# Kernel optimization log

Hardware: AMD Instinct MI355X
Metric: run time of the kernel (lower is better)

The kernel has to match this reference:

```python
import jax, jax.numpy as jnp
import numpy as np

B, S, HID = 2, 2048, 2048
NH, NKV, D = 32, 4, 64
N_REP = NH // NKV
EPS = 1e-6
ROPE_THETA = 10000.0


def _rotate_half(x):
    h = x.shape[-1] // 2
    return jnp.concatenate([-x[..., h:], x[..., :h]], axis=-1)


def _rmsnorm(x, gamma):
    # RMSNorm over last dim (head_dim)
    return x * jax.lax.rsqrt(jnp.mean(x * x, axis=-1, keepdims=True) + EPS) * gamma


def setup_inputs() -> dict:
    key = jax.random.key(0)
    ks = jax.random.split(key, 8)
    hidden_states = jax.random.normal(ks[0], (B, S, HID), dtype=jnp.float32)
    # rotary cos/sin tables, shape [B, S, D]
    pos = jnp.arange(S, dtype=jnp.float32)
    inv_freq = 1.0 / (ROPE_THETA ** (jnp.arange(0, D, 2, dtype=jnp.float32) / D))
    freqs = pos[:, None] * inv_freq[None, :]            # [S, D/2]
    emb = jnp.concatenate([freqs, freqs], axis=-1)      # [S, D]
    cos = jnp.broadcast_to(jnp.cos(emb)[None], (B, S, D))
    sin = jnp.broadcast_to(jnp.sin(emb)[None], (B, S, D))
    sc = 0.02
    Wq = jax.random.normal(ks[1], (NH * D, HID), dtype=jnp.float32) * sc
    Wk = jax.random.normal(ks[2], (NKV * D, HID), dtype=jnp.float32) * sc
    Wv = jax.random.normal(ks[3], (NKV * D, HID), dtype=jnp.float32) * sc
    Wg = jax.random.normal(ks[4], (NH * D, HID), dtype=jnp.float32) * sc
    Wo = jax.random.normal(ks[5], (HID, NH * D), dtype=jnp.float32) * sc
    q_gamma = jnp.ones((D,), dtype=jnp.float32)
    k_gamma = jnp.ones((D,), dtype=jnp.float32)
    return dict(hidden_states=hidden_states, cos=cos, sin=sin,
                Wq=Wq, Wk=Wk, Wv=Wv, Wg=Wg, Wo=Wo,
                q_gamma=q_gamma, k_gamma=k_gamma)


def reference(hidden_states, cos, sin, Wq, Wk, Wv, Wg, Wo, q_gamma, k_gamma):
    b, s, _ = hidden_states.shape
    q = (hidden_states @ Wq.T).reshape(b, s, NH, D)
    k = (hidden_states @ Wk.T).reshape(b, s, NKV, D)
    v = (hidden_states @ Wv.T).reshape(b, s, NKV, D)
    gate = hidden_states @ Wg.T                       # [B, S, NH*D]
    # per-head RMSNorm on q/k
    q = _rmsnorm(q, q_gamma)
    k = _rmsnorm(k, k_gamma)
    # [B, H, S, D]
    q = q.transpose(0, 2, 1, 3)
    k = k.transpose(0, 2, 1, 3)
    v = v.transpose(0, 2, 1, 3)
    # RoPE (unsqueeze_dim=1)
    c = cos[:, None, :, :]
    sn = sin[:, None, :, :]
    q = q * c + _rotate_half(q) * sn
    k = k * c + _rotate_half(k) * sn
    # GQA: repeat kv heads
    kr = jnp.repeat(k, N_REP, axis=1)
    vr = jnp.repeat(v, N_REP, axis=1)
    scaling = D ** -0.5
    scores = jnp.einsum('bhqd,bhkd->bhqk', q, kr) * scaling
    w = jax.nn.softmax(scores.astype(jnp.float32), axis=-1).astype(q.dtype)
    out = jnp.einsum('bhqk,bhkd->bhqd', w, vr)
    out = out.transpose(0, 2, 1, 3).reshape(b, s, NH * D)
    out = out * jax.nn.sigmoid(gate)
    return out @ Wo.T
```

## Files before the change

kernel.cpp:

```cpp
#include <hip/hip_runtime.h>


#define LOG2E 1.44269504088896340736f

typedef __attribute__((ext_vector_type(4))) float f32x4;
typedef __attribute__((ext_vector_type(8))) short bf16x8;

__device__ __forceinline__ float bf2f(unsigned short u) {
  union { unsigned u; float f; } x; x.u = ((unsigned)u) << 16; return x.f;
}
__device__ __forceinline__ unsigned short f2bf(float f) {
  union { float f; unsigned u; } x; x.f = f;
  unsigned r = x.u + 0x7fffu + ((x.u >> 16) & 1u);
  return (unsigned short)(r >> 16);
}

__device__ __forceinline__ void async16(void* lds, const void* g) {
  __builtin_amdgcn_global_load_lds(
      (const __attribute__((address_space(1))) unsigned*)g,
      (__attribute__((address_space(3))) unsigned*)lds, 16, 0, 0);
}
__device__ __forceinline__ void lds_fence() {
  __asm__ volatile("s_waitcnt lgkmcnt(0)" ::: "memory");
}

__global__ __launch_bounds__(256) void cvt_all(
    const float* __restrict__ s0, const float* __restrict__ s1,
    const float* __restrict__ s2, const float* __restrict__ s3,
    const float* __restrict__ s4, const float* __restrict__ s5,
    unsigned short* __restrict__ d0, unsigned short* __restrict__ d1,
    unsigned short* __restrict__ d2, unsigned short* __restrict__ d3,
    unsigned short* __restrict__ d4, unsigned short* __restrict__ d5) {
  long i = (long)blockIdx.x * 256 + threadIdx.x;
  const float* s; unsigned short* d; long off;
  if      (i < 2097152) { s = s0; d = d0; off = 0; }
  else if (i < 3145728) { s = s1; d = d1; off = 2097152; }
  else if (i < 3276800) { s = s2; d = d2; off = 3145728; }
  else if (i < 3407872) { s = s3; d = d3; off = 3276800; }
  else if (i < 4456448) { s = s4; d = d4; off = 3407872; }
  else                  { s = s5; d = d5; off = 4456448; }
  long j = i - off;
  float4 v = reinterpret_cast<const float4*>(s)[j];
  ushort4 u;
  u.x = f2bf(v.x); u.y = f2bf(v.y); u.z = f2bf(v.z); u.w = f2bf(v.w);
  reinterpret_cast<ushort4*>(d)[j] = u;
}

template <typename CT>
__device__ __forceinline__ void gemm128(
    const unsigned short* __restrict__ A, const unsigned short* __restrict__ W,
    CT* __restrict__ C, int m0, int n0, int ldc, int K,
    unsigned short* As, unsigned short* Bs) {
  const int tid = threadIdx.x;
  const int w = tid >> 6, l = tid & 63, quad = l >> 4, l16 = l & 15;
  const int wm = (w & 1) * 64, wn = (w >> 1) * 64;

  f32x4 acc[4][4];
  const f32x4 Z4 = {0.f, 0.f, 0.f, 0.f};
#pragma unroll
  for (int i = 0; i < 4; i++)
#pragma unroll
    for (int j = 0; j < 4; j++) acc[i][j] = Z4;

  const int srow = tid >> 2;
  const int scol = (tid & 3) * 8;
  const unsigned short* gA = A + (size_t)(m0 + srow) * K + scol;
  const unsigned short* gB = W + (size_t)(n0 + srow) * K + scol;
  unsigned short* lA = As + tid * 8;
  unsigned short* lB = Bs + tid * 8;

  for (int kb = 0; kb < K; kb += 32) {
    async16(lA,        gA + kb);
    async16(lA + 2048, gA + (size_t)64 * K + kb);
    async16(lB,        gB + kb);
    async16(lB + 2048, gB + (size_t)64 * K + kb);
    __syncthreads();

    bf16x8 af[4], bf[4];
#pragma unroll
    for (int mt = 0; mt < 4; mt++)
      af[mt] = *(const bf16x8*)&As[(wm + mt * 16 + l16) * 32 + quad * 8];
#pragma unroll
    for (int nt = 0; nt < 4; nt++)
      bf[nt] = *(const bf16x8*)&Bs[(wn + nt * 16 + l16) * 32 + quad * 8];
#pragma unroll
    for (int mt = 0; mt < 4; mt++)
#pragma unroll
      for (int nt = 0; nt < 4; nt++)
        acc[mt][nt] = __builtin_amdgcn_mfma_f32_16x16x32_bf16(
            af[mt], bf[nt], acc[mt][nt], 0, 0, 0);
    __syncthreads();
  }

#pragma unroll
  for (int mt = 0; mt < 4; mt++)
#pragma unroll
    for (int nt = 0; nt < 4; nt++) {
      int row = m0 + wm + mt * 16 + quad * 4;
      int col = n0 + wn + nt * 16 + l16;
#pragma unroll
      for (int r = 0; r < 4; r++) {
        if constexpr (sizeof(CT) == 2)
          C[(size_t)(row + r) * ldc + col] = f2bf(acc[mt][nt][r]);
        else
          C[(size_t)(row + r) * ldc + col] = acc[mt][nt][r];
      }
    }
}

__global__ __launch_bounds__(256) void gemm_qkvg(
    const unsigned short* __restrict__ X,
    const unsigned short* __restrict__ Wq, const unsigned short* __restrict__ Wk,
    const unsigned short* __restrict__ Wv, const unsigned short* __restrict__ Wg,
    unsigned short* __restrict__ Qr, unsigned short* __restrict__ Kr,
    unsigned short* __restrict__ Vr, unsigned short* __restrict__ Gr) {
  __shared__ __attribute__((aligned(16))) unsigned short As[128 * 32];
  __shared__ __attribute__((aligned(16))) unsigned short Bs[128 * 32];
  int ny = blockIdx.y;
  const unsigned short* W; unsigned short* C; int n0, ldc;
  if (ny < 16)      { W = Wq; C = Qr; n0 = ny * 128;        ldc = 2048; }
  else if (ny < 18) { W = Wk; C = Kr; n0 = (ny - 16) * 128; ldc = 256;  }
  else if (ny < 20) { W = Wv; C = Vr; n0 = (ny - 18) * 128; ldc = 256;  }
  else              { W = Wg; C = Gr; n0 = (ny - 20) * 128; ldc = 2048; }
  gemm128<unsigned short>(X, W, C, blockIdx.x * 128, n0, ldc, 2048, As, Bs);
}

__global__ __launch_bounds__(256) void gemm_out_k(
    const unsigned short* __restrict__ A, const unsigned short* __restrict__ W,
    float* __restrict__ C) {
  __shared__ __attribute__((aligned(16))) unsigned short As[128 * 32];
  __shared__ __attribute__((aligned(16))) unsigned short Bs[128 * 32];
  gemm128<float>(A, W, C, blockIdx.x * 128, blockIdx.y * 128, 2048, 2048, As, Bs);
}

__global__ __launch_bounds__(256) void prep_qkv(
    const unsigned short* __restrict__ Qr, const unsigned short* __restrict__ Kr,
    const unsigned short* __restrict__ Vr,
    const float* __restrict__ cosb, const float* __restrict__ sinb,
    const float* __restrict__ qg, const float* __restrict__ kg,
    unsigned short* __restrict__ Qn, unsigned short* __restrict__ Kn,
    unsigned short* __restrict__ Vt) {
  int idx = blockIdx.x * 4 + (threadIdx.x >> 6);
  int d = threadIdx.x & 63;
  int token = idx / 40;
  int unit = idx - token * 40;
  int b = token >> 11, s = token & 2047;

  if (unit >= 36) {
    int kvh = unit - 36;
    Vt[((size_t)(b * 4 + kvh) * 64 + d) * 2048 + s] =
        Vr[(size_t)token * 256 + kvh * 64 + d];
    return;
  }
  const unsigned short* src; const float* gamma; float scale; unsigned short* dst;
  if (unit < 32) {
    src = Qr + (size_t)token * 2048 + unit * 64;
    gamma = qg; scale = 0.125f;
    dst = Qn + ((size_t)(b * 32 + unit) * 2048 + s) * 64;
  } else {
    int kvh = unit - 32;
    src = Kr + (size_t)token * 256 + kvh * 64;
    gamma = kg; scale = LOG2E;
    dst = Kn + ((size_t)(b * 4 + kvh) * 2048 + s) * 64;
  }
  float x = bf2f(src[d]);
  float ss = x * x;
#pragma unroll
  for (int off = 32; off >= 1; off >>= 1) ss += __shfl_xor(ss, off);
  float rr = rsqrtf(ss * (1.0f / 64.0f) + 1e-6f);
  float xn = x * rr * gamma[d];
  float other = __shfl_xor(xn, 32);
  float rot = (d < 32) ? -other : other;
  size_t cs = (size_t)(b * 2048 + s) * 64 + d;
  dst[d] = f2bf((xn * cosb[cs] + rot * sinb[cs]) * scale);
}

__global__ __launch_bounds__(256, 4) void attn(
    const unsigned short* __restrict__ Qn, const unsigned short* __restrict__ Kn,
    const unsigned short* __restrict__ Vt, const unsigned short* __restrict__ gate,
    unsigned short* __restrict__ act) {
  __shared__ __attribute__((aligned(16))) unsigned short smem[20480];
  unsigned short* Ps = smem + 16384;

  const int tid = threadIdx.x, w = tid >> 6, l = tid & 63;
  const int quad = l >> 4, l16 = l & 15, l7 = l16 & 7;
  const int bh = blockIdx.y, b = bh >> 5, h = bh & 31, kvh = h >> 3;
  const int q0 = blockIdx.x * 128;

  const unsigned short* Qg = Qn + ((size_t)(b * 32 + h) * 2048 + q0) * 64;
  const unsigned short* Kg = Kn + (size_t)(b * 4 + kvh) * 2048 * 64;
  const unsigned short* Vg = Vt + (size_t)(b * 4 + kvh) * 64 * 2048;
  unsigned short* Pw = Ps + w * 1024;

  const int kq_src = ((tid & 7) ^ ((tid >> 3) & 7)) * 8;

#pragma unroll
  for (int i = 0; i < 4; i++)
    async16(smem + i * 2048 + tid * 8,
            Qg + (size_t)(i * 32 + (tid >> 3)) * 64 + kq_src);
  __syncthreads();
  bf16x8 qf[2][2];
#pragma unroll
  for (int mt = 0; mt < 2; mt++)
#pragma unroll
    for (int ks = 0; ks < 2; ks++) {
      int row = w * 32 + mt * 16 + l16;
      qf[mt][ks] = *(const bf16x8*)&smem[row * 64 + ((ks * 4 + quad) ^ l7) * 8];
    }
  __syncthreads();

  const f32x4 Z4 = {0.f, 0.f, 0.f, 0.f};
  f32x4 O[2][4];
  float lp[2][4];
#pragma unroll
  for (int mt = 0; mt < 2; mt++) {
#pragma unroll
    for (int nt = 0; nt < 4; nt++) O[mt][nt] = Z4;
#pragma unroll
    for (int r = 0; r < 4; r++) lp[mt][r] = 0.f;
  }

#pragma unroll
  for (int i = 0; i < 2; i++) {
    async16(smem + i * 2048 + tid * 8,
            Kg + (size_t)(i * 32 + (tid >> 3)) * 64 + kq_src);
    async16(smem + 4096 + i * 2048 + tid * 8,
            Vg + (size_t)(i * 32 + (tid >> 3)) * 2048 + kq_src);
  }

  for (int kt = 0; kt < 32; kt++) {
    __syncthreads();

    if (kt < 31) {
      unsigned short* nb = smem + ((kt + 1) & 1) * 8192;
      const int s1 = (kt + 1) * 64;
#pragma unroll
      for (int i = 0; i < 2; i++) {
        async16(nb + i * 2048 + tid * 8,
                Kg + (size_t)(s1 + i * 32 + (tid >> 3)) * 64 + kq_src);
        async16(nb + 4096 + i * 2048 + tid * 8,
                Vg + (size_t)(i * 32 + (tid >> 3)) * 2048 + s1 + kq_src);
      }
    }

    unsigned short* Ks  = smem + (kt & 1) * 8192;
    unsigned short* Vts = Ks + 4096;

    f32x4 sc[2][4];
#pragma unroll
    for (int mt = 0; mt < 2; mt++)
#pragma unroll
      for (int nt = 0; nt < 4; nt++) sc[mt][nt] = Z4;
#pragma unroll
    for (int nt = 0; nt < 4; nt++) {
      int row = nt * 16 + l16;
      bf16x8 kf0 = *(const bf16x8*)&Ks[row * 64 + (quad ^ l7) * 8];
      bf16x8 kf1 = *(const bf16x8*)&Ks[row * 64 + ((4 + quad) ^ l7) * 8];
#pragma unroll
      for (int mt = 0; mt < 2; mt++) {
        sc[mt][nt] = __builtin_amdgcn_mfma_f32_16x16x32_bf16(qf[mt][0], kf0, sc[mt][nt], 0, 0, 0);
        sc[mt][nt] = __builtin_amdgcn_mfma_f32_16x16x32_bf16(qf[mt][1], kf1, sc[mt][nt], 0, 0, 0);
      }
    }

#pragma unroll
    for (int ks2 = 0; ks2 < 2; ks2++) {
#pragma unroll
      for (int mt = 0; mt < 2; mt++)
#pragma unroll
        for (int ntl = 0; ntl < 2; ntl++) {
          int nt = ks2 * 2 + ntl;
#pragma unroll
          for (int r = 0; r < 4; r++) {
            float p = __builtin_amdgcn_exp2f(sc[mt][nt][r]);
            union { float f; unsigned u; } x; x.f = p;
            union { unsigned u; float f; } t; t.u = x.u & 0xffff0000u;
            lp[mt][r] += t.f;
            int q = mt * 16 + quad * 4 + r;
            int c = ntl * 2 + (l16 >> 3);
            int phys = c ^ ((q >> 1) & 3);
            Pw[q * 32 + phys * 8 + l7] = (unsigned short)(x.u >> 16);
          }
        }
      lds_fence();

      bf16x8 pf[2];
#pragma unroll
      for (int mt = 0; mt < 2; mt++) {
        int q = mt * 16 + l16;
        int phys = quad ^ ((l16 >> 1) & 3);
        pf[mt] = *(const bf16x8*)&Pw[q * 32 + phys * 8];
      }
#pragma unroll
      for (int nt2 = 0; nt2 < 4; nt2++) {
        int d = nt2 * 16 + l16;
        bf16x8 vf = *(const bf16x8*)&Vts[d * 64 + ((ks2 * 4 + quad) ^ l7) * 8];
#pragma unroll
        for (int mt = 0; mt < 2; mt++)
          O[mt][nt2] = __builtin_amdgcn_mfma_f32_16x16x32_bf16(
              pf[mt], vf, O[mt][nt2], 0, 0, 0);
      }
      lds_fence();
    }
  }

#pragma unroll
  for (int mt = 0; mt < 2; mt++)
#pragma unroll
    for (int r = 0; r < 4; r++) {
      float s = lp[mt][r];
#pragma unroll
      for (int off = 1; off < 16; off <<= 1) s += __shfl_xor(s, off);
      lp[mt][r] = s;
    }

#pragma unroll
  for (int mt = 0; mt < 2; mt++) {
    float inv[4];
#pragma unroll
    for (int r = 0; r < 4; r++) inv[r] = 1.0f / lp[mt][r];
#pragma unroll
    for (int nt = 0; nt < 4; nt++)
#pragma unroll
      for (int r = 0; r < 4; r++) {
        int srow = q0 + w * 32 + mt * 16 + quad * 4 + r;
        int col = h * 64 + nt * 16 + l16;
        size_t off = (size_t)(b * 2048 + srow) * 2048 + col;
        float g = bf2f(gate[off]);
        float sig = 1.0f / (1.0f + __builtin_amdgcn_exp2f(-g * LOG2E));
        act[off] = f2bf(O[mt][nt][r] * inv[r] * sig);
      }
  }
}

extern "C" void kernel_launch(void* const* d_in, const int* in_sizes, int n_in,
                              void* d_out, int out_size, void* d_ws, size_t ws_size,
                              hipStream_t stream) {
  const float* hid  = (const float*)d_in[0];
  const float* cosb = (const float*)d_in[1];
  const float* sinb = (const float*)d_in[2];
  const float* Wq   = (const float*)d_in[3];
  const float* Wk   = (const float*)d_in[4];
  const float* Wv   = (const float*)d_in[5];
  const float* Wg   = (const float*)d_in[6];
  const float* Wo   = (const float*)d_in[7];
  const float* qg   = (const float*)d_in[8];
  const float* kg   = (const float*)d_in[9];
  float* out = (float*)d_out;

  char* ws = (char*)d_ws;
  unsigned short* Xb   = (unsigned short*)(ws);
  unsigned short* WqB  = (unsigned short*)(ws + 16777216);
  unsigned short* WkB  = (unsigned short*)(ws + 25165824);
  unsigned short* WvB  = (unsigned short*)(ws + 26214400);
  unsigned short* WgB  = (unsigned short*)(ws + 27262976);
  unsigned short* WoB  = (unsigned short*)(ws + 35651584);
  unsigned short* Qraw = (unsigned short*)(ws + 44040192);
  unsigned short* Kraw = (unsigned short*)(ws + 60817408);
  unsigned short* Vraw = (unsigned short*)(ws + 62914560);
  unsigned short* gate = (unsigned short*)(ws + 65011712);
  unsigned short* Kn   = (unsigned short*)(ws + 81788928);
  unsigned short* Vt   = (unsigned short*)(ws + 83886080);
  unsigned short* Qn  = Xb;
  unsigned short* act = WqB;

  cvt_all<<<dim3(21504), dim3(256), 0, stream>>>(
      hid, Wq, Wk, Wv, Wg, Wo, Xb, WqB, WkB, WvB, WgB, WoB);

  gemm_qkvg<<<dim3(32, 36), dim3(256), 0, stream>>>(
      Xb, WqB, WkB, WvB, WgB, Qraw, Kraw, Vraw, gate);

  prep_qkv<<<dim3(40960), dim3(256), 0, stream>>>(
      Qraw, Kraw, Vraw, cosb, sinb, qg, kg, Qn, Kn, Vt);

  attn<<<dim3(16, 64), dim3(256), 0, stream>>>(Qn, Kn, Vt, gate, act);

  gemm_out_k<<<dim3(32, 16), dim3(256), 0, stream>>>(act, WoB, out);
}
```

Before: 411.3 us.

## Fuse RMSNorm, RoPE and V transpose into QKVG GEMM epilogue; swizzle LDS

Removes the separate prep_qkv kernel. The QKVG GEMM epilogue now applies per-head RMSNorm, RoPE and scaling to Q/K, writes V already transposed, and writes gate directly, using 16-lane shuffles inside the MFMA tile. This drops a full round trip of raw Q/K/V through global memory and one kernel launch. It also XOR-swizzles the LDS column layout in the shared GEMM mainloop to reduce bank conflicts. In exchange, the epilogue writes to the transposed V with scattered, strided stores, and it adds per-element cos/sin loads.

```diff
diff --git a/kernel.cpp b/kernel.cpp
--- a/kernel.cpp
+++ b/kernel.cpp
@@ -46,16 +46,14 @@
   reinterpret_cast<ushort4*>(d)[j] = u;
 }
 
-template <typename CT>
-__device__ __forceinline__ void gemm128(
+__device__ __forceinline__ void gemm_main(
     const unsigned short* __restrict__ A, const unsigned short* __restrict__ W,
-    CT* __restrict__ C, int m0, int n0, int ldc, int K,
-    unsigned short* As, unsigned short* Bs) {
+    int m0, int n0, int K, unsigned short* As, unsigned short* Bs,
+    f32x4 acc[4][4]) {
   const int tid = threadIdx.x;
   const int w = tid >> 6, l = tid & 63, quad = l >> 4, l16 = l & 15;
   const int wm = (w & 1) * 64, wn = (w >> 1) * 64;
 
-  f32x4 acc[4][4];
   const f32x4 Z4 = {0.f, 0.f, 0.f, 0.f};
 #pragma unroll
   for (int i = 0; i < 4; i++)
@@ -63,11 +61,12 @@
     for (int j = 0; j < 4; j++) acc[i][j] = Z4;
 
   const int srow = tid >> 2;
-  const int scol = (tid & 3) * 8;
+  const int scol = (((tid & 3) ^ ((tid >> 3) & 3))) * 8;
   const unsigned short* gA = A + (size_t)(m0 + srow) * K + scol;
   const unsigned short* gB = W + (size_t)(n0 + srow) * K + scol;
   unsigned short* lA = As + tid * 8;
   unsigned short* lB = Bs + tid * 8;
+  const int fsw = (quad ^ ((l16 >> 1) & 3)) * 8;
 
   for (int kb = 0; kb < K; kb += 32) {
     async16(lA,        gA + kb);
@@ -79,10 +78,10 @@
     bf16x8 af[4], bf[4];
 #pragma unroll
     for (int mt = 0; mt < 4; mt++)
-      af[mt] = *(const bf16x8*)&As[(wm + mt * 16 + l16) * 32 + quad * 8];
+      af[mt] = *(const bf16x8*)&As[(wm + mt * 16 + l16) * 32 + fsw];
 #pragma unroll
     for (int nt = 0; nt < 4; nt++)
-      bf[nt] = *(const bf16x8*)&Bs[(wn + nt * 16 + l16) * 32 + quad * 8];
+      bf[nt] = *(const bf16x8*)&Bs[(wn + nt * 16 + l16) * 32 + fsw];
 #pragma unroll
     for (int mt = 0; mt < 4; mt++)
 #pragma unroll
@@ -91,38 +90,100 @@
             af[mt], bf[nt], acc[mt][nt], 0, 0, 0);
     __syncthreads();
   }
-
-#pragma unroll
-  for (int mt = 0; mt < 4; mt++)
-#pragma unroll
-    for (int nt = 0; nt < 4; nt++) {
-      int row = m0 + wm + mt * 16 + quad * 4;
-      int col = n0 + wn + nt * 16 + l16;
-#pragma unroll
-      for (int r = 0; r < 4; r++) {
-        if constexpr (sizeof(CT) == 2)
-          C[(size_t)(row + r) * ldc + col] = f2bf(acc[mt][nt][r]);
-        else
-          C[(size_t)(row + r) * ldc + col] = acc[mt][nt][r];
-      }
-    }
 }
 
 __global__ __launch_bounds__(256) void gemm_qkvg(
     const unsigned short* __restrict__ X,
     const unsigned short* __restrict__ Wq, const unsigned short* __restrict__ Wk,
     const unsigned short* __restrict__ Wv, const unsigned short* __restrict__ Wg,
-    unsigned short* __restrict__ Qr, unsigned short* __restrict__ Kr,
-    unsigned short* __restrict__ Vr, unsigned short* __restrict__ Gr) {
+    const float* __restrict__ cosb, const float* __restrict__ sinb,
+    const float* __restrict__ qg, const float* __restrict__ kg,
+    unsigned short* __restrict__ Qn, unsigned short* __restrict__ Kn,
+    unsigned short* __restrict__ Vt, unsigned short* __restrict__ gate) {
   __shared__ __attribute__((aligned(16))) unsigned short As[128 * 32];
   __shared__ __attribute__((aligned(16))) unsigned short Bs[128 * 32];
-  int ny = blockIdx.y;
-  const unsigned short* W; unsigned short* C; int n0, ldc;
-  if (ny < 16)      { W = Wq; C = Qr; n0 = ny * 128;        ldc = 2048; }
-  else if (ny < 18) { W = Wk; C = Kr; n0 = (ny - 16) * 128; ldc = 256;  }
-  else if (ny < 20) { W = Wv; C = Vr; n0 = (ny - 18) * 128; ldc = 256;  }
-  else              { W = Wg; C = Gr; n0 = (ny - 20) * 128; ldc = 2048; }
-  gemm128<unsigned short>(X, W, C, blockIdx.x * 128, n0, ldc, 2048, As, Bs);
+  const int ny = blockIdx.y;
+  const unsigned short* W; int n0, type;
+  if (ny < 16)      { W = Wq; n0 = ny * 128;        type = 0; }
+  else if (ny < 18) { W = Wk; n0 = (ny - 16) * 128; type = 1; }
+  else if (ny < 20) { W = Wv; n0 = (ny - 18) * 128; type = 2; }
+  else              { W = Wg; n0 = (ny - 20) * 128; type = 3; }
+  const int m0 = blockIdx.x * 128;
+
+  f32x4 acc[4][4];
+  gemm_main(X, W, m0, n0, 2048, As, Bs, acc);
+
+  const int tid = threadIdx.x;
+  const int w = tid >> 6, l = tid & 63, quad = l >> 4, l16 = l & 15;
+  const int wm = (w & 1) * 64, wn = (w >> 1) * 64;
+
+  if (type == 3) {
+#pragma unroll
+    for (int mt = 0; mt < 4; mt++)
+#pragma unroll
+      for (int r = 0; r < 4; r++) {
+        int row = m0 + wm + mt * 16 + quad * 4 + r;
+#pragma unroll
+        for (int nt = 0; nt < 4; nt++)
+          gate[(size_t)row * 2048 + n0 + wn + nt * 16 + l16] =
+              f2bf(acc[mt][nt][r]);
+      }
+    return;
+  }
+  if (type == 2) {
+#pragma unroll
+    for (int mt = 0; mt < 4; mt++)
+#pragma unroll
+      for (int r = 0; r < 4; r++) {
+        int row = m0 + wm + mt * 16 + quad * 4 + r;
+        int b = row >> 11, s = row & 2047;
+#pragma unroll
+        for (int nt = 0; nt < 4; nt++) {
+          int col = n0 + wn + nt * 16 + l16;
+          int kvh = col >> 6, d = col & 63;
+          Vt[((size_t)(b * 4 + kvh) * 64 + d) * 2048 + s] =
+              f2bf(acc[mt][nt][r]);
+        }
+      }
+    return;
+  }
+
+  const float* gamma = (type == 0) ? qg : kg;
+  const float scale  = (type == 0) ? 0.125f : LOG2E;
+  const int hb = (n0 + wn) >> 6;
+  float gv[4];
+#pragma unroll
+  for (int nt = 0; nt < 4; nt++) gv[nt] = gamma[nt * 16 + l16];
+
+#pragma unroll
+  for (int mt = 0; mt < 4; mt++)
+#pragma unroll
+    for (int r = 0; r < 4; r++) {
+      int row = m0 + wm + mt * 16 + quad * 4 + r;
+      float ss = 0.f;
+#pragma unroll
+      for (int nt = 0; nt < 4; nt++) {
+        float v = acc[mt][nt][r]; ss += v * v;
+      }
+#pragma unroll
+      for (int off = 1; off < 16; off <<= 1) ss += __shfl_xor(ss, off);
+      float rr = rsqrtf(ss * (1.0f / 64.0f) + 1e-6f);
+      float xn[4];
+#pragma unroll
+      for (int nt = 0; nt < 4; nt++) xn[nt] = acc[mt][nt][r] * rr * gv[nt];
+      int b = row >> 11, s = row & 2047;
+      unsigned short* dst = (type == 0)
+          ? Qn + ((size_t)(b * 32 + hb) * 2048 + s) * 64
+          : Kn + ((size_t)(b * 4 + hb) * 2048 + s) * 64;
+#pragma unroll
+      for (int nt = 0; nt < 4; nt++) {
+        int d = nt * 16 + l16;
+        float rot = (nt < 2) ? -xn[nt ^ 2] : xn[nt ^ 2];
+        float cv = cosb[(size_t)row * 64 + d];
+        float sv = sinb[(size_t)row * 64 + d];
+        dst[d] = f2bf((xn[nt] * cv + rot * sv) * scale);
+      }
+    }
 }
 
 __global__ __launch_bounds__(256) void gemm_out_k(
@@ -130,49 +191,22 @@
     float* __restrict__ C) {
   __shared__ __attribute__((aligned(16))) unsigned short As[128 * 32];
   __shared__ __attribute__((aligned(16))) unsigned short Bs[128 * 32];
-  gemm128<float>(A, W, C, blockIdx.x * 128, blockIdx.y * 128, 2048, 2048, As, Bs);
-}
-
-__global__ __launch_bounds__(256) void prep_qkv(
-    const unsigned short* __restrict__ Qr, const unsigned short* __restrict__ Kr,
-    const unsigned short* __restrict__ Vr,
-    const float* __restrict__ cosb, const float* __restrict__ sinb,
-    const float* __restrict__ qg, const float* __restrict__ kg,
-    unsigned short* __restrict__ Qn, unsigned short* __restrict__ Kn,
-    unsigned short* __restrict__ Vt) {
-  int idx = blockIdx.x * 4 + (threadIdx.x >> 6);
-  int d = threadIdx.x & 63;
-  int token = idx / 40;
-  int unit = idx - token * 40;
-  int b = token >> 11, s = token & 2047;
-
-  if (unit >= 36) {
-    int kvh = unit - 36;
-    Vt[((size_t)(b * 4 + kvh) * 64 + d) * 2048 + s] =
-        Vr[(size_t)token * 256 + kvh * 64 + d];
-    return;
-  }
-  const unsigned short* src; const float* gamma; float scale; unsigned short* dst;
-  if (unit < 32) {
-    src = Qr + (size_t)token * 2048 + unit * 64;
-    gamma = qg; scale = 0.125f;
-    dst = Qn + ((size_t)(b * 32 + unit) * 2048 + s) * 64;
-  } else {
-    int kvh = unit - 32;
-    src = Kr + (size_t)token * 256 + kvh * 64;
-    gamma = kg; scale = LOG2E;
-    dst = Kn + ((size_t)(b * 4 + kvh) * 2048 + s) * 64;
-  }
-  float x = bf2f(src[d]);
-  float ss = x * x;
-#pragma unroll
-  for (int off = 32; off >= 1; off >>= 1) ss += __shfl_xor(ss, off);
-  float rr = rsqrtf(ss * (1.0f / 64.0f) + 1e-6f);
-  float xn = x * rr * gamma[d];
-  float other = __shfl_xor(xn, 32);
-  float rot = (d < 32) ? -other : other;
-  size_t cs = (size_t)(b * 2048 + s) * 64 + d;
-  dst[d] = f2bf((xn * cosb[cs] + rot * sinb[cs]) * scale);
+  const int m0 = blockIdx.x * 128, n0 = blockIdx.y * 128;
+  f32x4 acc[4][4];
+  gemm_main(A, W, m0, n0, 2048, As, Bs, acc);
+  const int tid = threadIdx.x;
+  const int w = tid >> 6, l = tid & 63, quad = l >> 4, l16 = l & 15;
+  const int wm = (w & 1) * 64, wn = (w >> 1) * 64;
+#pragma unroll
+  for (int mt = 0; mt < 4; mt++)
+#pragma unroll
+    for (int nt = 0; nt < 4; nt++) {
+      int row = m0 + wm + mt * 16 + quad * 4;
+      int col = n0 + wn + nt * 16 + l16;
+#pragma unroll
+      for (int r = 0; r < 4; r++)
+        C[(size_t)(row + r) * 2048 + col] = acc[mt][nt][r];
+    }
 }
 
 __global__ __launch_bounds__(256, 4) void attn(
@@ -355,23 +389,17 @@
   unsigned short* WvB  = (unsigned short*)(ws + 26214400);
   unsigned short* WgB  = (unsigned short*)(ws + 27262976);
   unsigned short* WoB  = (unsigned short*)(ws + 35651584);
-  unsigned short* Qraw = (unsigned short*)(ws + 44040192);
-  unsigned short* Kraw = (unsigned short*)(ws + 60817408);
-  unsigned short* Vraw = (unsigned short*)(ws + 62914560);
-  unsigned short* gate = (unsigned short*)(ws + 65011712);
-  unsigned short* Kn   = (unsigned short*)(ws + 81788928);
-  unsigned short* Vt   = (unsigned short*)(ws + 83886080);
-  unsigned short* Qn  = Xb;
+  unsigned short* gate = (unsigned short*)(ws + 44040192);
+  unsigned short* Qn   = (unsigned short*)(ws + 60817408);
+  unsigned short* Kn   = (unsigned short*)(ws + 77594624);
+  unsigned short* Vt   = (unsigned short*)(ws + 79691776);
   unsigned short* act = WqB;
 
   cvt_all<<<dim3(21504), dim3(256), 0, stream>>>(
       hid, Wq, Wk, Wv, Wg, Wo, Xb, WqB, WkB, WvB, WgB, WoB);
 
   gemm_qkvg<<<dim3(32, 36), dim3(256), 0, stream>>>(
-      Xb, WqB, WkB, WvB, WgB, Qraw, Kraw, Vraw, gate);
-
-  prep_qkv<<<dim3(40960), dim3(256), 0, stream>>>(
-      Qraw, Kraw, Vraw, cosb, sinb, qg, kg, Qn, Kn, Vt);
+      Xb, WqB, WkB, WvB, WgB, cosb, sinb, qg, kg, Qn, Kn, Vt, gate);
 
   attn<<<dim3(16, 64), dim3(256), 0, stream>>>(Qn, Kn, Vt, gate, act);
 
```

Result: faster. 392.7 us (-4.5%).
